# Optimization experiments

Hardware: AMD Instinct MI355X
Metric: run time of the kernel (lower is better)

Reference implementation:

```python
import jax, jax.numpy as jnp
import numpy as np

LEAK = 0.2

def leaky(x):
    return jnp.where(x > 0, x, LEAK * x)

def relu(x):
    return jnp.maximum(x, 0)

def conv1d(x, w):
    # x [B,Cin,L], w [Cout,Cin,3], stride 1, padding 1
    return jax.lax.conv_general_dilated(x, w, (1,), [(1, 1)],
        dimension_numbers=('NCH', 'OIH', 'NCH'))

def conv2d(x, w, pad, dil=1, groups=1):
    return jax.lax.conv_general_dilated(x, w, (1, 1), [(pad, pad), (pad, pad)],
        rhs_dilation=(dil, dil), feature_group_count=groups,
        dimension_numbers=('NCHW', 'OIHW', 'NCHW'))

def bn2d(x, p, eps=1e-5):
    # p: [4,C] = gamma, beta, running_mean, running_var (eval-mode BN)
    g, b, m, v = p
    s = (1, -1, 1, 1)
    return (x - m.reshape(s)) * (g.reshape(s) / jnp.sqrt(v.reshape(s) + eps)) + b.reshape(s)

def layernorm(x, g, b, eps=1e-5):
    mu = x.mean(-1, keepdims=True)
    var = ((x - mu) ** 2).mean(-1, keepdims=True)
    return (x - mu) / jnp.sqrt(var + eps) * g + b

def l2n(x, axis, eps):
    n = jnp.sqrt((x * x).sum(axis, keepdims=True))
    return x / jnp.maximum(n, eps)


def setup_inputs() -> dict:
    key = jax.random.key(0)
    B, C, H, W = 4, 64, 48, 48
    D, Fn, T, V = 256, 8, 4, 16
    E = 16  # orthogonal prototype embed dim
    ks = iter(jax.random.split(key, 64))
    def rn(shape, s=0.05):
        return jax.random.normal(next(ks), shape, jnp.float32) * s
    def bnp(c):
        return jnp.stack([1.0 + rn((c,), 0.1), rn((c,), 0.1), rn((c,), 0.1), 1.0 + jnp.abs(rn((c,), 0.1))])
    return dict(
        basis_vector_bank=jax.random.normal(next(ks), (T, V, D), jnp.float32),
        task_f=jax.random.normal(next(ks), (B, C, 16, 16), jnp.float32),
        img_f=jax.random.normal(next(ks), (B, C, H, W), jnp.float32),
        protos=jax.random.normal(next(ks), (T, E), jnp.float32),
        tA_w1=rn((E // 4, 1, 3)), tA_w2=rn((E // 2, E // 4, 3)),
        iA_w=rn((E // 2, C, 3, 3)), iA_bn=bnp(E // 2),
        at_w1=rn((E, Fn // 2 * E)), at_b1=rn((Fn // 2 * E,)),
        at_ln_g=jnp.ones((Fn // 2 * E,)), at_ln_b=jnp.zeros((Fn // 2 * E,)),
        at_w2=rn((Fn // 2 * E, Fn * E)), at_b2=rn((Fn * E,)),
        bv_t1=rn((D // 4, 1, 3)), bv_t2=rn((D // 2, D // 4, 3)),
        bv_ic1=rn((D // 4, C, 3, 3)), bv_bn1=bnp(D // 4),
        bv_ic2=rn((D // 2, D // 4, 3, 3)), bv_bn2=bnp(D // 2),
        bv_w1=rn((D, D // 4)), bv_b1=rn((D // 4,)),
        bv_ln_g=jnp.ones((D // 4,)), bv_ln_b=jnp.zeros((D // 4,)),
        bv_w2=rn((D // 4, D)), bv_b2=rn((D,)),
        m1_w1=rn((D, D // 4)), m1_b1=rn((D // 4,)),
        m1_ln_g=jnp.ones((D // 4,)), m1_ln_b=jnp.zeros((D // 4,)),
        m1_w2=rn((D // 4, C * C)), m1_b2=rn((C * C,)),
        m3_w1=rn((D, D // 4)), m3_b1=rn((D // 4,)),
        m3_ln_g=jnp.ones((D // 4,)), m3_ln_b=jnp.zeros((D // 4,)),
        m3_w2=rn((D // 4, 9 * C * C)), m3_b2=rn((9 * C * C,)),
        blr_bn=bnp(C),
        zc_w=rn((C, C, 1, 1), 0.01), zc_b=rn((C,), 0.01),
    )


def _forward(basis_vector_bank, task_f, img_f, protos, tA_w1, tA_w2, iA_w, iA_bn,
             at_w1, at_b1, at_ln_g, at_ln_b, at_w2, at_b2,
             bv_t1, bv_t2, bv_ic1, bv_bn1, bv_ic2, bv_bn2,
             bv_w1, bv_b1, bv_ln_g, bv_ln_b, bv_w2, bv_b2,
             m1_w1, m1_b1, m1_ln_g, m1_ln_b, m1_w2, m1_b2,
             m3_w1, m3_b1, m3_ln_g, m3_ln_b, m3_w2, m3_b2,
             blr_bn, zc_w, zc_b):
    T, V, D = basis_vector_bank.shape
    B, C, H, W = img_f.shape
    E = protos.shape[1]
    Fn = at_w2.shape[1] // E
    tau = 0.5

    # --- A2SI routing features ---
    xt = task_f.reshape(B, 1, -1)
    t1 = conv1d(leaky(conv1d(xt, tA_w1)), tA_w2).mean(-1)          # [B,E/2]
    i1 = leaky(bn2d(conv2d(img_f, iA_w, 1), iA_bn)).mean((2, 3))   # [B,E/2]
    f1 = jnp.concatenate([t1, i1], axis=1)                         # [B,E]
    h = relu(layernorm(f1 @ at_w1 + at_b1, at_ln_g, at_ln_b))
    tif = (h @ at_w2 + at_b2).reshape(B, E, Fn)                    # [B,E,F]
    logits = jnp.einsum('te,bef->bft', l2n(protos, -1, 1e-8), l2n(tif, 1, 1e-8))  # [B,F,T]

    # hard gumbel-softmax (straight-through), fixed noise key for determinism
    u = jax.random.uniform(jax.random.key(42), logits.shape, jnp.float32, 1e-10, 1.0)
    g = -jnp.log(-jnp.log(u))
    y = jax.nn.softmax((logits + g) / tau, axis=-1)
    idx = jnp.argmax(y, axis=-1)                                   # [B,F]
    y_hard = jax.nn.one_hot(idx, T, dtype=y.dtype)
    set_type = y_hard + y - jax.lax.stop_gradient(y)

    bank_flat = basis_vector_bank.reshape(T, V * D)
    sbvb = jnp.einsum('bft,tk->bfk', set_type, bank_flat).reshape(B, Fn, V, D)

    # --- BasisV_filter: filter feature ---
    xt2 = task_f.reshape(B, C, -1)
    rms = jnp.sqrt((xt2 ** 2).mean((1, 2), keepdims=True))
    xt2 = (xt2 / (rms + 1e-8)).reshape(B, 1, -1)
    te = conv1d(leaky(conv1d(xt2, bv_t1)), bv_t2).mean(-1)         # [B,D/2]
    ie = leaky(bn2d(conv2d(img_f, bv_ic1, 1), bv_bn1))
    ie = leaky(bn2d(conv2d(ie, bv_ic2, 1), bv_bn2)).mean((2, 3))   # [B,D/2]
    ff = jnp.concatenate([te, ie], axis=1)                         # [B,D]
    ff = relu(layernorm(ff @ bv_w1 + bv_b1, bv_ln_g, bv_ln_b)) @ bv_w2 + bv_b2

    # --- per-(batch,type) group gather/top-k/scatter, vectorized ---
    # group bank = bank of first filter with that type (hard one-hot -> type's bank)
    occ = idx[:, None, :] == jnp.arange(T)[None, :, None]          # [B,T,F]
    first = jnp.argmax(occ, axis=-1)                               # [B,T]
    Bg = jnp.take_along_axis(sbvb, first[:, :, None, None], axis=1)  # [B,T,V,D]
    # all rows of Q within a group are identical (filter_f expanded over F),
    # so S.max(0) == cosine(ff[b], Bg[b,t])
    scores = jnp.einsum('bd,btvd->btv', l2n(ff, -1, 1e-12), l2n(Bg, -1, 1e-12))
    order = jnp.argsort(-scores, axis=-1)                          # [B,T,V] topk order
    lt = jnp.tril(jnp.ones((Fn, Fn), bool), -1)                    # j < i
    rank = ((idx[:, :, None] == idx[:, None, :]) & lt).sum(-1)     # position in group
    bidx = jnp.arange(B)[:, None]
    sel = order[bidx, idx, rank]                                   # [B,F]
    bvf = Bg[bidx, idx, sel]                                       # [B,F,D]

    # --- per-filter dynamic convolutions ---
    w1 = relu(layernorm(bvf @ m1_w1 + m1_b1, m1_ln_g, m1_ln_b)) @ m1_w2 + m1_b2
    w1 = w1.reshape(B, Fn, C, C)                                   # [B,F,out,in]
    w3 = relu(layernorm(bvf @ m3_w1 + m3_b1, m3_ln_g, m3_ln_b)) @ m3_w2 + m3_b2
    w3 = w3.reshape(B * Fn, C, C, 3, 3)

    dp0 = jnp.einsum('bfoc,bchw->bfohw', w1, img_f)                # 1x1 branch
    xin = jnp.broadcast_to(img_f[:, None], (B, Fn, C, H, W)).reshape(1, B * Fn * C, H, W)
    ker = w3.reshape(B * Fn * C, C, 3, 3)
    dpd = [conv2d(xin, ker, d, dil=d, groups=B * Fn).reshape(B, Fn, C, H, W)
           for d in (1, 2, 3)]                                     # same-padded dilated 3x3
    t_ = idx[:, :, None, None, None]
    dp = jnp.where(t_ == 0, dp0, jnp.where(t_ == 1, dpd[0],
         jnp.where(t_ == 2, dpd[1], dpd[2])))                      # [B,F,C,H,W]

    x = leaky(bn2d(dp.reshape(B * Fn, C, H, W), blr_bn)).reshape(B, Fn, C, H, W).mean(1)
    a = conv2d(x, zc_w, 0) + zc_b.reshape(1, -1, 1, 1)
    return a + img_f


@jax.jit
def reference(basis_vector_bank, task_f, img_f, protos, tA_w1, tA_w2, iA_w, iA_bn,
              at_w1, at_b1, at_ln_g, at_ln_b, at_w2, at_b2,
              bv_t1, bv_t2, bv_ic1, bv_bn1, bv_ic2, bv_bn2,
              bv_w1, bv_b1, bv_ln_g, bv_ln_b, bv_w2, bv_b2,
              m1_w1, m1_b1, m1_ln_g, m1_ln_b, m1_w2, m1_b2,
              m3_w1, m3_b1, m3_ln_g, m3_ln_b, m3_w2, m3_b2,
              blr_bn, zc_w, zc_b):
    return _forward(basis_vector_bank, task_f, img_f, protos, tA_w1, tA_w2, iA_w, iA_bn,
                    at_w1, at_b1, at_ln_g, at_ln_b, at_w2, at_b2,
                    bv_t1, bv_t2, bv_ic1, bv_bn1, bv_ic2, bv_bn2,
                    bv_w1, bv_b1, bv_ln_g, bv_ln_b, bv_w2, bv_b2,
                    m1_w1, m1_b1, m1_ln_g, m1_ln_b, m1_w2, m1_b2,
                    m3_w1, m3_b1, m3_ln_g, m3_ln_b, m3_w2, m3_b2,
                    blr_bn, zc_w, zc_b)
```

## Files before the change

kernel.cpp:

```cpp
#include <hip/hip_runtime.h>
#include <math.h>

#define LEAKC 0.2f

#define NB 4
#define NC 64
#define LLEN 16384
#define HW 2304
#define PP 54
#define PHW 2916
#define SLABP 72
#define CP 72
#define IE1C 50

typedef __attribute__((ext_vector_type(8))) short short8;
typedef __attribute__((ext_vector_type(4))) float floatx4;

__device__ __forceinline__ float leaky(float x){ return x > 0.f ? x : LEAKC*x; }

__device__ __forceinline__ float wave_sum64(float v){
  for(int off=32;off;off>>=1) v += __shfl_xor(v,off);
  return v;
}

__device__ __forceinline__ unsigned short f2bf(float x){
  unsigned u=__float_as_uint(x);
  unsigned r=u+0x7FFFu+((u>>16)&1u);
  return (unsigned short)(r>>16);
}

__device__ __forceinline__ void threefry2x32(unsigned k0, unsigned k1, unsigned& x0, unsigned& x1){
  unsigned ks0=k0, ks1=k1, ks2=k0^k1^0x1BD11BDAu;
  x0+=ks0; x1+=ks1;
  const int rot0[4]={13,15,26,6};
  const int rot1[4]={17,29,16,24};
#define TF_APPLY(rr) {for(int r=0;r<4;r++){x0+=x1; x1=(x1<<rr[r])|(x1>>(32-rr[r])); x1^=x0;}}
  TF_APPLY(rot0); x0+=ks1; x1+=ks2+1u;
  TF_APPLY(rot1); x0+=ks2; x1+=ks0+2u;
  TF_APPLY(rot0); x0+=ks0; x1+=ks1+3u;
  TF_APPLY(rot1); x0+=ks1; x1+=ks2+4u;
  TF_APPLY(rot0); x0+=ks2; x1+=ks0+5u;
#undef TF_APPLY
}

__device__ __forceinline__ float jax_uniform128(int i){
  unsigned x0=0u, x1=(unsigned)i;
  threefry2x32(0u,42u,x0,x1);
  unsigned bits = x0 ^ x1;
  unsigned fb=(bits>>9)|0x3f800000u;
  float f=__uint_as_float(fb)-1.0f;
  float u=f*(1.0f-1e-10f)+1e-10f;
  return fmaxf(1e-10f,u);
}

__global__ __launch_bounds__(256) void k_pre(const float* __restrict__ task_f,
                      const float* __restrict__ w1A, const float* __restrict__ w1B,
                      float* __restrict__ totApart, float* __restrict__ a0A, float* __restrict__ aLA,
                      float* __restrict__ totBpart, float* __restrict__ a0B, float* __restrict__ aLB,
                      float* __restrict__ rmspart,
                      const float* __restrict__ img,
                      const float* __restrict__ w1, const float* __restrict__ w2,
                      const float* __restrict__ wa,
                      unsigned short* __restrict__ imgTP,
                      unsigned short* __restrict__ W1T, unsigned short* __restrict__ W2T,
                      unsigned short* __restrict__ WAT,
                      const float* __restrict__ mw1, const float* __restrict__ mw3,
                      const float* __restrict__ bvw1p, const float* __restrict__ bvw2p,
                      const float* __restrict__ bvt2p, const float* __restrict__ atw2p,
                      const float* __restrict__ bankp, float* __restrict__ warm){
  if(blockIdx.x<256){
    int b=blockIdx.x>>6, seg=blockIdx.x&63;
    const float* x=task_f+b*LLEN;
    float tA[4]={0,0,0,0};
    float tB[64];
#pragma unroll
    for(int c=0;c<64;c++) tB[c]=0.f;
    float sq=0.f;
    int l=seg*256+threadIdx.x;
    {
      float xm=(l>0)?x[l-1]:0.f;
      float xc=x[l];
      float xp=(l<LLEN-1)?x[l+1]:0.f;
      sq=xc*xc;
#pragma unroll
      for(int c=0;c<4;c++){
        float a=leaky(w1A[c*3+0]*xm + w1A[c*3+1]*xc + w1A[c*3+2]*xp);
        tA[c]=a;
        if(l==0) a0A[b*4+c]=a;
        if(l==LLEN-1) aLA[b*4+c]=a;
      }
#pragma unroll
      for(int c=0;c<64;c++){
        float a=leaky(w1B[c*3+0]*xm + w1B[c*3+1]*xc + w1B[c*3+2]*xp);
        tB[c]=a;
        if(l==0) a0B[b*64+c]=a;
        if(l==LLEN-1) aLB[b*64+c]=a;
      }
    }
    sq=wave_sum64(sq);
#pragma unroll
    for(int c=0;c<4;c++) tA[c]=wave_sum64(tA[c]);
#pragma unroll
    for(int c=0;c<64;c++){
      float v=tB[c];
      for(int off=32;off;off>>=1) v+=__shfl_down(v,off);
      tB[c]=v;
    }
    __shared__ float redB[4][64];
    __shared__ float redA[4][4];
    __shared__ float redQ[4];
    int wave=threadIdx.x>>6, lane=threadIdx.x&63;
    if(lane==0){
#pragma unroll
      for(int c=0;c<64;c++) redB[wave][c]=tB[c];
#pragma unroll
      for(int c=0;c<4;c++) redA[wave][c]=tA[c];
      redQ[wave]=sq;
    }
    __syncthreads();
    if(threadIdx.x<64){
      float s=redB[0][threadIdx.x]+redB[1][threadIdx.x]+redB[2][threadIdx.x]+redB[3][threadIdx.x];
      totBpart[(size_t)(b*64+seg)*64+threadIdx.x]=s;
    } else if(threadIdx.x<68){
      int c=threadIdx.x-64;
      totApart[(b*64+seg)*4+c]=redA[0][c]+redA[1][c]+redA[2][c]+redA[3][c];
    } else if(threadIdx.x==68){
      rmspart[b*64+seg]=redQ[0]+redQ[1]+redQ[2]+redQ[3];
    }
  } else if(blockIdx.x<400){
    int blk=blockIdx.x-256;
    int b=blk/36, t=blk%36;
    int p0=t*64;
    __shared__ float tile[64][65];
    int pp=threadIdx.x&63, c4=threadIdx.x>>6;
    for(int r=0;r<16;r++){
      int c=c4*16+r;
      tile[c][pp]=img[(b*64+c)*HW + p0+pp];
    }
    __syncthreads();
    int pxl=threadIdx.x>>2, cg=(threadIdx.x&3)*16;
    unsigned out[8];
#pragma unroll
    for(int q=0;q<8;q++){
      unsigned lo=f2bf(tile[cg+2*q][pxl]);
      unsigned hi=f2bf(tile[cg+2*q+1][pxl]);
      out[q]=lo|(hi<<16);
    }
    int px=p0+pxl;
    int h=px/48, w=px-h*48;
    int poff=(h+3)*PP+(w+3);
    unsigned* dst=(unsigned*)(imgTP + ((size_t)(b*PHW+poff))*64 + cg);
#pragma unroll
    for(int q=0;q<8;q++) dst[q]=out[q];
  } else if(blockIdx.x<868){
    int n=(blockIdx.x-400)*256+threadIdx.x;
    if(n<9*64*64){
      int tap=n>>12, oc=(n>>6)&63, c=n&63;
      W1T[n]=f2bf(w1[oc*576+c*9+tap]);
    } else if(n<9*64*64+9*128*64){
      int m=n-9*64*64;
      int tap=m/8192, r=m-tap*8192, oc=r>>6, c=r&63;
      W2T[m]=f2bf(w2[oc*576+c*9+tap]);
    } else {
      int q=n-9*64*64-9*128*64;
      if(q<9*16*64){
        int tap=q>>10, r=q&1023, o=r>>6, c=r&63;
        WAT[q]=(o<8)?f2bf(wa[o*576+c*9+tap]):(unsigned short)0;
      }
    }
  } else if(blockIdx.x<884){
    int t=(blockIdx.x-868)*256+threadIdx.x;
    float a=0.f;
    for(int i=t;i*16<16384;i+=4096) a+=mw1[i*16];
    for(int i=t;i*16<16384;i+=4096) a+=mw3[i*16];
    for(int i=t;i*16<16384;i+=4096) a+=bvw1p[i*16];
    for(int i=t;i*16<16384;i+=4096) a+=bvw2p[i*16];
    for(int i=t;i*16<24576;i+=4096) a+=bvt2p[i*16];
    for(int i=t;i*16<8192;i+=4096) a+=atw2p[i*16];
    for(int i=t;i*16<16384;i+=4096) a+=bankp[i*16];
    warm[t&1023]=a;
  } else {
    int id=(blockIdx.x-884)*256+threadIdx.x;
    uint4 z=make_uint4(0,0,0,0);
    for(int cch=id;cch<19584;cch+=4096){
      int ck=cch&7, pxid=cch>>3;
      int b=pxid/612, p=pxid-b*612;
      int h,w;
      if(p<324){ int r=p/54; w=p-r*54; h=(r<3)?r:(r+48); }
      else { int q=p-324; int r2=q/6; int cc=q-r2*6; h=3+r2; w=(cc<3)?cc:(cc+48); }
      *(uint4*)(imgTP + ((size_t)(b*PHW + h*PP + w))*64 + ck*8)=z;
    }
  }
}

__global__ __launch_bounds__(512) void k_conv12(const unsigned short* __restrict__ imgTP,
                        const unsigned short* __restrict__ W1T,
                        const unsigned short* __restrict__ W2T,
                        const unsigned short* __restrict__ WAT,
                        const float* __restrict__ bn1, const float* __restrict__ bn2,
                        const float* __restrict__ bnA,
                        float* __restrict__ iepart, float* __restrict__ i1part){
  int tid=threadIdx.x;
  int lane=tid&63, wv=tid>>6;
  int n0=lane&15, kg=lane>>4;
  if(blockIdx.x<96){
    int blk=blockIdx.x;
    int b=blk/24, hp=blk-b*24;
    int h0=hp*2;
    __shared__ unsigned short slab[6*54*SLABP];
    __shared__ unsigned short ie1[4*IE1C*CP];
    {
      const unsigned short* ibase=imgTP+((size_t)b*PHW+(size_t)(h0+1)*PP)*64;
      for(int e=tid;e<6*54*8;e+=512){
        int rr=e/(54*8), rem=e-rr*54*8, w=rem>>3, ck=rem&7;
        uint4 v=*(const uint4*)(ibase+((size_t)(rr*PP+w))*64+ck*8);
        *(uint4*)(slab+(rr*54+w)*SLABP+ck*8)=v;
      }
      if(tid<64){
        int br=tid>>4, cq=(tid>>3)&1, ck=tid&7;
        *(uint4*)(ie1+((size_t)(br*IE1C+(cq?49:0)))*CP+ck*8)=make_uint4(0,0,0,0);
      }
    }
    __syncthreads();
    {
      int mt=wv&3, rh=wv>>2;
      floatx4 acc[2][3];
#pragma unroll
      for(int rr=0;rr<2;rr++)
#pragma unroll
        for(int nt=0;nt<3;nt++) acc[rr][nt]=(floatx4){0.f,0.f,0.f,0.f};
#pragma unroll
      for(int ti=0;ti<3;ti++){
#pragma unroll
        for(int tj=0;tj<3;tj++){
          int tap=ti*3+tj;
          const unsigned short* Ab=W1T+(size_t)tap*4096;
#pragma unroll
          for(int c0=0;c0<64;c0+=32){
            short8 a=*(const short8*)(Ab+((mt*16+n0)*64+c0+kg*8));
#pragma unroll
            for(int rr=0;rr<2;rr++){
              int sr=rh*2+rr+ti;
#pragma unroll
              for(int nt=0;nt<3;nt++){
                int sc=nt*16+n0+tj+2;
                short8 bv=*(const short8*)(slab+(sr*54+sc)*SLABP+c0+kg*8);
                acc[rr][nt]=__builtin_amdgcn_mfma_f32_16x16x32_bf16(a,bv,acc[rr][nt],0,0,0);
              }
            }
          }
        }
      }
      int obase=mt*16+kg*4;
      float scale[4],m_[4],be_[4];
#pragma unroll
      for(int reg=0;reg<4;reg++){
        int o=obase+reg;
        scale[reg]=bn1[o]/sqrtf(bn1[192+o]+1e-5f);
        m_[reg]=bn1[128+o]; be_[reg]=bn1[64+o];
      }
#pragma unroll
      for(int rr=0;rr<2;rr++){
        int br=rh*2+rr;
        bool rv=((unsigned)(h0-1+br))<48u;
#pragma unroll
        for(int nt=0;nt<3;nt++){
          float v0=rv?leaky((acc[rr][nt][0]-m_[0])*scale[0]+be_[0]):0.f;
          float v1=rv?leaky((acc[rr][nt][1]-m_[1])*scale[1]+be_[1]):0.f;
          float v2=rv?leaky((acc[rr][nt][2]-m_[2])*scale[2]+be_[2]):0.f;
          float v3=rv?leaky((acc[rr][nt][3]-m_[3])*scale[3]+be_[3]):0.f;
          unsigned w0=f2bf(v0)|((unsigned)f2bf(v1)<<16);
          unsigned w1=f2bf(v2)|((unsigned)f2bf(v3)<<16);
          uint2 pk={w0,w1};
          *(uint2*)(ie1+((size_t)(br*IE1C+(nt*16+1+n0)))*CP+obase)=pk;
        }
      }
    }
    __syncthreads();
    {
      int mt2=wv;
      floatx4 acc[6];
#pragma unroll
      for(int i=0;i<6;i++) acc[i]=(floatx4){0.f,0.f,0.f,0.f};
#pragma unroll
      for(int ti=0;ti<3;ti++){
#pragma unroll
        for(int tj=0;tj<3;tj++){
          int tap=ti*3+tj;
          const unsigned short* Ab=W2T+(size_t)tap*8192;
#pragma unroll
          for(int c0=0;c0<64;c0+=32){
            short8 a=*(const short8*)(Ab+((mt2*16+n0)*64+c0+kg*8));
#pragma unroll
            for(int rr=0;rr<2;rr++){
              int sr=rr+ti;
#pragma unroll
              for(int wc=0;wc<3;wc++){
                int q=wc*16+n0+tj;
                short8 bv=*(const short8*)(ie1+((size_t)(sr*IE1C+q))*CP+c0+kg*8);
                acc[rr*3+wc]=__builtin_amdgcn_mfma_f32_16x16x32_bf16(a,bv,acc[rr*3+wc],0,0,0);
              }
            }
          }
        }
      }
      int obase=mt2*16+kg*4;
#pragma unroll
      for(int reg=0;reg<4;reg++){
        int o=obase+reg;
        float scale=bn2[o]/sqrtf(bn2[384+o]+1e-5f);
        float m_=bn2[256+o], be_=bn2[128+o];
        float part=0;
#pragma unroll
        for(int i=0;i<6;i++) part+=leaky((acc[i][reg]-m_)*scale+be_);
        for(int off=1;off<16;off<<=1) part+=__shfl_xor(part,off);
        if(n0==0) iepart[(b*24+hp)*128+o]=part*(1.f/2304.f);
      }
    }
  } else {
    int blk2=blockIdx.x-96;
    int b=blk2/3, hg=blk2-b*3;
    int hp=hg*8+wv;
    int h0=hp*2;
    const unsigned short* ib=imgTP+(size_t)b*PHW*64;
    floatx4 acc[6];
#pragma unroll
    for(int i=0;i<6;i++) acc[i]=(floatx4){0.f,0.f,0.f,0.f};
#pragma unroll
    for(int ti=0;ti<3;ti++){
#pragma unroll
      for(int tj=0;tj<3;tj++){
        int tap=ti*3+tj;
        const unsigned short* Ab=WAT+(size_t)tap*1024;
#pragma unroll
        for(int c0=0;c0<64;c0+=32){
          short8 a=*(const short8*)(Ab+(n0*64+c0+kg*8));
#pragma unroll
          for(int rr=0;rr<2;rr++){
            int r=h0+rr+ti-1+3;
#pragma unroll
            for(int wc=0;wc<3;wc++){
              int w=wc*16+n0+tj-1+3;
              short8 bv=*(const short8*)(ib+((size_t)(r*PP+w)*64+c0+kg*8));
              acc[rr*3+wc]=__builtin_amdgcn_mfma_f32_16x16x32_bf16(a,bv,acc[rr*3+wc],0,0,0);
            }
          }
        }
      }
    }
    int obase=kg*4;
#pragma unroll
    for(int reg=0;reg<4;reg++){
      int o=obase+reg;
      float part=0;
      if(o<8){
        float scale=bnA[o]/sqrtf(bnA[24+o]+1e-5f);
        float m_=bnA[16+o], be_=bnA[8+o];
#pragma unroll
        for(int i=0;i<6;i++) part+=leaky((acc[i][reg]-m_)*scale+be_);
      }
      for(int off=1;off<16;off<<=1) part+=__shfl_xor(part,off);
      if(n0==0 && o<8) i1part[(b*24+hp)*8+o]=part*(1.f/2304.f);
    }
  }
}

__global__ __launch_bounds__(512,1) void k_mid(
    const float* __restrict__ totApart, const float* __restrict__ a0A, const float* __restrict__ aLA,
    const float* __restrict__ totBpart, const float* __restrict__ a0B, const float* __restrict__ aLB,
    const float* __restrict__ rmspart,
    const float* __restrict__ tA_w2, const float* __restrict__ bv_t2,
    const float* __restrict__ i1part, const float* __restrict__ iepart,
    const float* __restrict__ at_w1, const float* __restrict__ at_b1,
    const float* __restrict__ at_ln_g, const float* __restrict__ at_ln_b,
    const float* __restrict__ at_w2, const float* __restrict__ at_b2,
    const float* __restrict__ protos,
    const float* __restrict__ bv_w1, const float* __restrict__ bv_b1,
    const float* __restrict__ bv_ln_g, const float* __restrict__ bv_ln_b,
    const float* __restrict__ bv_w2, const float* __restrict__ bv_b2,
    const float* __restrict__ bank,
    const float* __restrict__ m1_w1, const float* __restrict__ m1_b1,
    const float* __restrict__ m1_g,  const float* __restrict__ m1_bb,
    const float* __restrict__ m3_w1, const float* __restrict__ m3_b1,
    const float* __restrict__ m3_g,  const float* __restrict__ m3_bb,
    int* __restrict__ idxo, float* __restrict__ hid1, float* __restrict__ hid3){
  int b=blockIdx.x;
  int tid=threadIdx.x;
  int lane=tid&63, wv=tid>>6;
  const float invL=1.0f/16384.0f;
  __shared__ float sT[64], s0[64], sL[64];
  __shared__ float totA_s[4];
  __shared__ float rms_s;
  __shared__ float part[512];
  __shared__ float te_s[128], t1_s[8];
  __shared__ float f1[16], h[64], tif[128], tifn[128], tden[8], pden[4], pn[64], z[32];
  __shared__ int sidx[8], sfirst[4], srank[8], rows[8];
  __shared__ float fbuf[256], hh[64], ffn_s[256], finv_s;
  __shared__ float scores[64];
  __shared__ int order[64];
  __shared__ float bvf[2048];

  if(tid<64){
    float s=0;
#pragma unroll 8
    for(int seg=0;seg<64;seg++) s+=totBpart[(size_t)(b*64+seg)*64+tid];
    sT[tid]=s;
  } else if(tid<128){
    int t=tid-64;
    s0[t]=a0B[b*64+t]; sL[t]=aLB[b*64+t];
  } else if(tid<192){
    float v=rmspart[b*64+(tid-128)];
    v=wave_sum64(v);
    if(tid==128) rms_s=v;
  } else if(tid<256){
    int c=tid-192;
    if(c<4){
      float s=0;
#pragma unroll 8
      for(int seg=0;seg<64;seg++) s+=totApart[(b*64+seg)*4+c];
      totA_s[c]=s;
    }
  }
  __syncthreads();
  float scB=1.0f/(sqrtf(rms_s*invL)+1e-8f);
  if(tid<256){
    int c2=tid&127, h2=tid>>7;
    const float* wr=bv_t2+c2*192;
    float s=0;
    for(int c1=h2*32;c1<h2*32+32;c1+=8){
      float4 q[6];
      const float4* r4=(const float4*)(wr+c1*3);
#pragma unroll
      for(int u=0;u<6;u++) q[u]=r4[u];
      const float* qq=(const float*)q;
#pragma unroll
      for(int u=0;u<8;u++){
        int c=c1+u;
        float T=sT[c], A0=s0[c], AL=sL[c];
        s += qq[u*3+0]*(T-AL) + qq[u*3+1]*T + qq[u*3+2]*(T-A0);
      }
    }
    part[tid]=s;
  } else if(tid>=384 && tid<392){
    int c2=tid-384;
    float s=0;
    for(int c1=0;c1<4;c1++){
      float T=totA_s[c1], A0=a0A[b*4+c1], AL=aLA[b*4+c1];
      const float* w=&tA_w2[(c2*4+c1)*3];
      s += w[0]*(T-AL) + w[1]*T + w[2]*(T-A0);
    }
    t1_s[c2]=s*invL;
  }
  __syncthreads();
  if(tid<128) te_s[tid]=(part[tid]+part[tid+128])*invL*scB;
  __syncthreads();

  if(tid<8) f1[tid]=t1_s[tid];
  else if(tid<16){
    int f=tid-8;
    float s=0;
#pragma unroll
    for(int g=0;g<24;g++) s+=i1part[(b*24+g)*8+f];
    f1[tid]=s;
  }
  __syncthreads();
  if(tid<64){
    float s=at_b1[lane];
#pragma unroll
    for(int i=0;i<16;i++) s+=f1[i]*at_w1[i*64+lane];
    float mu=wave_sum64(s)*(1.f/64.f);
    float d=s-mu;
    float var=wave_sum64(d*d)*(1.f/64.f);
    h[lane]=fmaxf(d*(1.0f/sqrtf(var+1e-5f))*at_ln_g[lane]+at_ln_b[lane],0.f);
  }
  __syncthreads();
  if(tid<256){
    int n=tid&127, h2=tid>>7;
    float a0=0,a1=0;
    for(int k=h2*32;k<h2*32+32;k+=2){
      a0+=h[k]*at_w2[k*128+n];
      a1+=h[k+1]*at_w2[(k+1)*128+n];
    }
    part[tid]=a0+a1;
  }
  __syncthreads();
  if(tid<128) tif[tid]=at_b2[tid]+part[tid]+part[tid+128];
  __syncthreads();
  if(tid<8){
    int f=tid;
    float ss=0; for(int e=0;e<16;e++){float v=tif[e*8+f]; ss+=v*v;}
    tden[f]=fmaxf(sqrtf(ss),1e-8f);
  } else if(tid<12){
    int t=tid-8;
    float ss=0; for(int e=0;e<16;e++){float v=protos[t*16+e]; ss+=v*v;}
    pden[t]=fmaxf(sqrtf(ss),1e-8f);
  }
  __syncthreads();
  if(tid<128) tifn[tid]=tif[tid]/tden[tid&7];
  if(tid<64) pn[tid]=protos[tid]/pden[tid>>4];
  __syncthreads();
  if(tid<32){
    int f=tid>>2, t=tid&3;
    float ss=0;
#pragma unroll
    for(int e=0;e<16;e++) ss+=pn[t*16+e]*tifn[e*8+f];
    float u=jax_uniform128(b*32+f*4+t);
    float g=-logf(-logf(u));
    z[tid]=ss+g;
  }
  __syncthreads();
  if(tid<8){
    float best=z[tid*4]; int bi=0;
    for(int t=1;t<4;t++){ float v=z[tid*4+t]; if(v>best){best=v;bi=t;} }
    sidx[tid]=bi;
  }
  __syncthreads();
  if(tid<4){
    int t=tid;
    int fi=0;
    for(int f=7;f>=0;f--) if(sidx[f]==t) fi=f;
    sfirst[t]=fi;
  } else if(tid<12){
    int f=tid-4;
    int c=0; for(int f2=0;f2<f;f2++) if(sidx[f2]==sidx[f]) c++;
    srank[f]=c;
  }
  __syncthreads();

  if(tid<128) fbuf[tid]=te_s[tid];
  else if(tid<256){
    int c=tid-128;
    float s=0;
#pragma unroll 8
    for(int g=0;g<24;g++) s+=iepart[(b*24+g)*128+c];
    fbuf[tid]=s;
  }
  __syncthreads();
  if(tid<256){
    int l64=tid&63, q=tid>>6;
    float a0=0,a1=0,a2=0,a3=0;
    for(int k=q*64;k<q*64+64;k+=4){
      a0+=fbuf[k]  *bv_w1[k*64+l64];
      a1+=fbuf[k+1]*bv_w1[(k+1)*64+l64];
      a2+=fbuf[k+2]*bv_w1[(k+2)*64+l64];
      a3+=fbuf[k+3]*bv_w1[(k+3)*64+l64];
    }
    part[tid]=((a0+a1)+(a2+a3));
  }
  __syncthreads();
  if(tid<64){
    float s=bv_b1[lane]+part[lane]+part[64+lane]+part[128+lane]+part[192+lane];
    float mu=wave_sum64(s)*(1.f/64.f);
    float d=s-mu;
    float var=wave_sum64(d*d)*(1.f/64.f);
    hh[lane]=fmaxf(d*(1.0f/sqrtf(var+1e-5f))*bv_ln_g[lane]+bv_ln_b[lane],0.f);
  }
  __syncthreads();
  {
    int n=tid&255, h2=tid>>8;
    float a0=0,a1=0;
    for(int k=h2*32;k<h2*32+32;k+=2){
      a0+=hh[k]*bv_w2[k*256+n];
      a1+=hh[k+1]*bv_w2[(k+1)*256+n];
    }
    part[tid]=a0+a1;
  }
  __syncthreads();
  if(tid<256) ffn_s[tid]=bv_b2[tid]+part[tid]+part[tid+256];
  __syncthreads();
  if(tid<64){
    float sq=0;
#pragma unroll
    for(int u=0;u<4;u++){ float v=ffn_s[u*64+lane]; sq+=v*v; }
    sq=wave_sum64(sq);
    if(lane==0) finv_s=1.0f/fmaxf(sqrtf(sq),1e-12f);
  }
  __syncthreads();
  if(tid<256) ffn_s[tid]*=finv_s;
  __syncthreads();

  if(tid<128){
    int it=tid&63, h2=tid>>6;
    int t=it>>4, v=it&15;
    int tt=sidx[sfirst[t]];
    const float4* row=(const float4*)(bank+(tt*16+v)*256);
    float sa=0,na=0;
    for(int d4=h2*32;d4<h2*32+32;d4++){
      float4 r=row[d4];
      const float* fp=&ffn_s[d4*4];
      sa+=fp[0]*r.x+fp[1]*r.y+fp[2]*r.z+fp[3]*r.w;
      na+=r.x*r.x+r.y*r.y+r.z*r.z+r.w*r.w;
    }
    part[tid]=sa;
    part[256+tid]=na;
  }
  __syncthreads();
  if(tid<64) scores[tid]=(part[tid]+part[tid+64])/fmaxf(sqrtf(part[256+tid]+part[320+tid]),1e-12f);
  __syncthreads();
  if(tid<4){
    const float* sc=&scores[tid*16];
    unsigned used=0;
    for(int pk=0;pk<16;pk++){
      int best=-1; float bv=-1e30f;
      for(int v2=0;v2<16;v2++){
        if(used&(1u<<v2)) continue;
        float vv=sc[v2];
        if(best<0||vv>bv){bv=vv;best=v2;}
      }
      used|=1u<<best;
      order[tid*16+pk]=best;
    }
  }
  __syncthreads();
  if(tid<8){
    int t=sidx[tid];
    int v=order[t*16+srank[tid]];
    rows[tid]=t*16+v;
    idxo[b*8+tid]=t;
  }
  __syncthreads();

  for(int ii=tid;ii<2048;ii+=512){
    int r=ii>>8, d=ii&255;
    bvf[ii]=bank[rows[r]*256+d];
  }
  __syncthreads();
  {
    int r=wv;
    const float* bp=&bvf[r*256];
    float a0=0,a1=0,a2=0,a3=0;
    float c0=0,c1=0,c2=0,c3=0;
    for(int d=0;d<256;d+=4){
      float b0=bp[d],b1=bp[d+1],b2=bp[d+2],b3=bp[d+3];
      a0+=b0*m1_w1[d*64+lane];
      a1+=b1*m1_w1[(d+1)*64+lane];
      a2+=b2*m1_w1[(d+2)*64+lane];
      a3+=b3*m1_w1[(d+3)*64+lane];
      c0+=b0*m3_w1[d*64+lane];
      c1+=b1*m3_w1[(d+1)*64+lane];
      c2+=b2*m3_w1[(d+2)*64+lane];
      c3+=b3*m3_w1[(d+3)*64+lane];
    }
    float s1=m1_b1[lane]+((a0+a1)+(a2+a3));
    float s3=m3_b1[lane]+((c0+c1)+(c2+c3));
    float mu=wave_sum64(s1)*(1.f/64.f);
    float dd=s1-mu;
    float var=wave_sum64(dd*dd)*(1.f/64.f);
    hid1[(b*8+r)*64+lane]=fmaxf(dd*(1.0f/sqrtf(var+1e-5f))*m1_g[lane]+m1_bb[lane],0.f);
    mu=wave_sum64(s3)*(1.f/64.f);
    dd=s3-mu;
    var=wave_sum64(dd*dd)*(1.f/64.f);
    hid3[(b*8+r)*64+lane]=fmaxf(dd*(1.0f/sqrtf(var+1e-5f))*m3_g[lane]+m3_bb[lane],0.f);
  }
}

__global__ __launch_bounds__(256) void k_heads(const float* __restrict__ hid1, const float* __restrict__ hid3,
                        const float* __restrict__ w2a, const float* __restrict__ b2a,
                        const float* __restrict__ w2b, const float* __restrict__ b2b,
                        unsigned short* __restrict__ A1, unsigned short* __restrict__ A3){
  __shared__ float hl[2048];
  if(blockIdx.x<16){
    int n=blockIdx.x*256+threadIdx.x;
    for(int i=threadIdx.x;i<2048;i+=256) hl[i]=hid1[i];
    __syncthreads();
    float wcol[64];
#pragma unroll
    for(int k=0;k<64;k++) wcol[k]=w2a[k*4096+n];
    float bb=b2a[n];
    for(int bf=0;bf<32;bf++){
      float s=bb;
#pragma unroll
      for(int k=0;k<64;k++) s+=hl[bf*64+k]*wcol[k];
      A1[bf*4096+n]=f2bf(s);
    }
  } else {
    int n=(blockIdx.x-16)*256+threadIdx.x;
    for(int i=threadIdx.x;i<2048;i+=256) hl[i]=hid3[i];
    __syncthreads();
    float wcol[64];
#pragma unroll
    for(int k=0;k<64;k++) wcol[k]=w2b[(size_t)k*36864+n];
    float bb=b2b[n];
    int o=n/576, rem=n-o*576;
    int c=rem/9, tap=rem-c*9;
    size_t base=((size_t)tap*64+o)*64+c;
    for(int bf=0;bf<32;bf++){
      float s=bb;
#pragma unroll
      for(int k=0;k<64;k++) s+=hl[bf*64+k]*wcol[k];
      A3[(size_t)bf*9*4096+base]=f2bf(s);
    }
  }
}

__global__ __launch_bounds__(512) void k_dynF(const unsigned short* __restrict__ imgTP,
                       const unsigned short* __restrict__ A1, const unsigned short* __restrict__ A3,
                       const int* __restrict__ idx, const float* __restrict__ bn,
                       const float* __restrict__ zc_w, const float* __restrict__ zc_b,
                       const float* __restrict__ img, float* __restrict__ out){
  int blk=blockIdx.x;
  int b=blk/48, r0=blk-b*48;
  int tid=threadIdx.x;
  int lane=tid&63, w8=tid>>6;
  int mt=w8&3, fh=w8>>2;
  int n0=lane&15, kg=lane>>4;
  __shared__ unsigned short slab[7*54*SLABP];
  __shared__ float xl[64*50];
  __shared__ float zl[4096];
  for(int i=tid;i<4096;i+=512) zl[i]=zc_w[i];
  for(int i=tid;i<3200;i+=512) xl[i]=0.f;
  {
    const unsigned short* ibase=imgTP+((size_t)b*PHW+(size_t)r0*PP)*64;
    for(int e=tid;e<7*54*8;e+=512){
      int rr=e/(54*8), rem=e-rr*54*8, w=rem>>3, ck=rem&7;
      uint4 v=*(const uint4*)(ibase + ((size_t)(rr*PP+w))*64 + ck*8);
      *(uint4*)(slab + (rr*54+w)*SLABP + ck*8)=v;
    }
  }
  __syncthreads();
  int obase=mt*16+kg*4;
  float scale[4],m_[4],be_[4];
#pragma unroll
  for(int reg=0;reg<4;reg++){
    int o=obase+reg;
    scale[reg]=bn[o]/sqrtf(bn[192+o]+1e-5f);
    m_[reg]=bn[128+o]; be_[reg]=bn[64+o];
  }
  float xsum[3][4];
#pragma unroll
  for(int wc=0;wc<3;wc++)
#pragma unroll
    for(int reg=0;reg<4;reg++) xsum[wc][reg]=0.f;
  for(int f=fh*4;f<fh*4+4;f++){
    int bf=b*8+f;
    int tt=idx[bf];
    floatx4 acc[3];
#pragma unroll
    for(int i=0;i<3;i++) acc[i]=(floatx4){0.f,0.f,0.f,0.f};
    if(tt==0){
      const unsigned short* Ab=A1+(size_t)bf*4096;
#pragma unroll
      for(int c0=0;c0<64;c0+=32){
        short8 a=*(const short8*)(Ab+((mt*16+n0)*64+c0+kg*8));
#pragma unroll
        for(int wc=0;wc<3;wc++){
          short8 bv=*(const short8*)(slab + (3*54 + wc*16+n0+3)*SLABP + c0+kg*8);
          acc[wc]=__builtin_amdgcn_mfma_f32_16x16x32_bf16(a,bv,acc[wc],0,0,0);
        }
      }
    } else {
      int d=tt;
      const unsigned short* A3b=A3+(size_t)bf*9*4096;
#pragma unroll
      for(int ti=0;ti<3;ti++){
        int lr=d*(ti-1)+3;
#pragma unroll
        for(int tj=0;tj<3;tj++){
          int tap=ti*3+tj;
          int dw=d*(tj-1)+3;
          const unsigned short* Ab=A3b+(size_t)tap*4096;
#pragma unroll
          for(int c0=0;c0<64;c0+=32){
            short8 a=*(const short8*)(Ab+((mt*16+n0)*64+c0+kg*8));
#pragma unroll
            for(int wc=0;wc<3;wc++){
              short8 bv=*(const short8*)(slab + (lr*54 + wc*16+n0+dw)*SLABP + c0+kg*8);
              acc[wc]=__builtin_amdgcn_mfma_f32_16x16x32_bf16(a,bv,acc[wc],0,0,0);
            }
          }
        }
      }
    }
#pragma unroll
    for(int wc=0;wc<3;wc++)
#pragma unroll
      for(int reg=0;reg<4;reg++)
        xsum[wc][reg]+=leaky((acc[wc][reg]-m_[reg])*scale[reg]+be_[reg]);
  }
#pragma unroll
  for(int wc=0;wc<3;wc++)
#pragma unroll
    for(int reg=0;reg<4;reg++)
      atomicAdd(&xl[(obase+reg)*50 + wc*16+n0], xsum[wc][reg]*0.125f);
  __syncthreads();
  size_t base=(size_t)b*64*HW + r0*48;
  for(int e=tid;e<3072;e+=512){
    int o=e/48, px=e-o*48;
    float s=zc_b[o];
#pragma unroll
    for(int c=0;c<64;c++) s+=zl[o*64+c]*xl[c*50+px];
    size_t a=base+(size_t)o*HW+px;
    out[a]=s+img[a];
  }
}

extern "C" void kernel_launch(void* const* d_in, const int* in_sizes, int n_in,
                              void* d_out, int out_size, void* d_ws, size_t ws_size,
                              hipStream_t stream){
  const float* bank   =(const float*)d_in[0];
  const float* task_f =(const float*)d_in[1];
  const float* img_f  =(const float*)d_in[2];
  const float* protos =(const float*)d_in[3];
  const float* tA_w1  =(const float*)d_in[4];
  const float* tA_w2  =(const float*)d_in[5];
  const float* iA_w   =(const float*)d_in[6];
  const float* iA_bn  =(const float*)d_in[7];
  const float* at_w1  =(const float*)d_in[8];
  const float* at_b1  =(const float*)d_in[9];
  const float* at_ln_g=(const float*)d_in[10];
  const float* at_ln_b=(const float*)d_in[11];
  const float* at_w2  =(const float*)d_in[12];
  const float* at_b2  =(const float*)d_in[13];
  const float* bv_t1  =(const float*)d_in[14];
  const float* bv_t2  =(const float*)d_in[15];
  const float* bv_ic1 =(const float*)d_in[16];
  const float* bv_bn1 =(const float*)d_in[17];
  const float* bv_ic2 =(const float*)d_in[18];
  const float* bv_bn2 =(const float*)d_in[19];
  const float* bv_w1  =(const float*)d_in[20];
  const float* bv_b1  =(const float*)d_in[21];
  const float* bv_ln_g=(const float*)d_in[22];
  const float* bv_ln_b=(const float*)d_in[23];
  const float* bv_w2  =(const float*)d_in[24];
  const float* bv_b2  =(const float*)d_in[25];
  const float* m1_w1  =(const float*)d_in[26];
  const float* m1_b1  =(const float*)d_in[27];
  const float* m1_ln_g=(const float*)d_in[28];
  const float* m1_ln_b=(const float*)d_in[29];
  const float* m1_w2  =(const float*)d_in[30];
  const float* m1_b2  =(const float*)d_in[31];
  const float* m3_w1  =(const float*)d_in[32];
  const float* m3_b1  =(const float*)d_in[33];
  const float* m3_ln_g=(const float*)d_in[34];
  const float* m3_ln_b=(const float*)d_in[35];
  const float* m3_w2  =(const float*)d_in[36];
  const float* m3_b2  =(const float*)d_in[37];
  const float* blr_bn =(const float*)d_in[38];
  const float* zc_w   =(const float*)d_in[39];
  const float* zc_b   =(const float*)d_in[40];

  float* ws=(float*)d_ws;
  float* totApart=ws+0;
  float* a0A  =ws+1024;
  float* aLA  =ws+1040;
  float* totBpart=ws+1056;
  float* a0B  =ws+17440;
  float* aLB  =ws+17696;
  float* rmspart=ws+17952;
  float* i1part =ws+18208;
  float* iepart =ws+18976;
  int*   idxp   =(int*)(ws+31264);
  float* hid1=ws+31296;
  float* hid3=ws+33344;
  unsigned short* A1p  =(unsigned short*)(ws+35392);
  unsigned short* A3p  =(unsigned short*)(ws+100928);
  unsigned short* imgTP=(unsigned short*)(ws+690752);
  unsigned short* W1Tp =(unsigned short*)(ws+1064000);
  unsigned short* W2Tp =(unsigned short*)(ws+1082432);
  unsigned short* WATp =(unsigned short*)(ws+1119296);
  float* warm =ws+1123904;

  k_pre<<<900,256,0,stream>>>(task_f, tA_w1, bv_t1,
                              totApart, a0A, aLA, totBpart, a0B, aLB, rmspart,
                              img_f, bv_ic1, bv_ic2, iA_w, imgTP, W1Tp, W2Tp, WATp,
                              m1_w1, m3_w1, bv_w1, bv_w2, bv_t2, at_w2, bank, warm);
  k_conv12<<<108,512,0,stream>>>(imgTP, W1Tp, W2Tp, WATp, bv_bn1, bv_bn2, iA_bn,
                                 iepart, i1part);
  k_mid<<<4,512,0,stream>>>(totApart,a0A,aLA,totBpart,a0B,aLB, rmspart, tA_w2, bv_t2,
                            i1part, iepart,
                            at_w1, at_b1, at_ln_g, at_ln_b, at_w2, at_b2, protos,
                            bv_w1, bv_b1, bv_ln_g, bv_ln_b, bv_w2, bv_b2, bank,
                            m1_w1, m1_b1, m1_ln_g, m1_ln_b,
                            m3_w1, m3_b1, m3_ln_g, m3_ln_b,
                            idxp, hid1, hid3);
  k_heads<<<160,256,0,stream>>>(hid1, hid3, m1_w2, m1_b2, m3_w2, m3_b2, A1p, A3p);
  k_dynF<<<192,512,0,stream>>>(imgTP, A1p, A3p, idxp, blr_bn, zc_w, zc_b, img_f, (float*)d_out);

  (void)in_sizes; (void)n_in; (void)out_size; (void)ws_size;
}
```

Measured before the change: 267.2 us.

## Fuse preprocessing and conv kernels into one launch, converting weights inline

Merges the preprocessing kernel and the conv12 kernel into a single 512-thread kernel. The conv blocks now read img_f directly and convert it to a bf16 slab in shared memory, instead of reading the transposed imgTP buffer. Conv weights are converted from fp32 to bf16 on the fly inside the MFMA loops rather than pre-transposed in a separate pass. The iA conv is computed from the shared slab within the same blocks, with partials expanded to 6 per block. This removes one launch and the weight-transpose pass, at the cost of strided fp32 weight gathers and conversions in the inner loops. Both the pre and conv work now run in one grid, so the conv blocks no longer depend on imgTP.

```diff
diff --git a/kernel.cpp b/kernel.cpp
--- a/kernel.cpp
+++ b/kernel.cpp
@@ -53,30 +53,36 @@
   return fmaxf(1e-10f,u);
 }
 
-__global__ __launch_bounds__(256) void k_pre(const float* __restrict__ task_f,
-                      const float* __restrict__ w1A, const float* __restrict__ w1B,
-                      float* __restrict__ totApart, float* __restrict__ a0A, float* __restrict__ aLA,
-                      float* __restrict__ totBpart, float* __restrict__ a0B, float* __restrict__ aLB,
-                      float* __restrict__ rmspart,
-                      const float* __restrict__ img,
-                      const float* __restrict__ w1, const float* __restrict__ w2,
-                      const float* __restrict__ wa,
-                      unsigned short* __restrict__ imgTP,
-                      unsigned short* __restrict__ W1T, unsigned short* __restrict__ W2T,
-                      unsigned short* __restrict__ WAT,
-                      const float* __restrict__ mw1, const float* __restrict__ mw3,
-                      const float* __restrict__ bvw1p, const float* __restrict__ bvw2p,
-                      const float* __restrict__ bvt2p, const float* __restrict__ atw2p,
-                      const float* __restrict__ bankp, float* __restrict__ warm){
-  if(blockIdx.x<256){
-    int b=blockIdx.x>>6, seg=blockIdx.x&63;
+__global__ __launch_bounds__(512) void kP(
+    const float* __restrict__ task_f,
+    const float* __restrict__ w1A, const float* __restrict__ w1B,
+    float* __restrict__ totApart, float* __restrict__ a0A, float* __restrict__ aLA,
+    float* __restrict__ totBpart, float* __restrict__ a0B, float* __restrict__ aLB,
+    float* __restrict__ rmspart,
+    const float* __restrict__ img,
+    const float* __restrict__ w1, const float* __restrict__ w2, const float* __restrict__ wa,
+    unsigned short* __restrict__ imgTP,
+    const float* __restrict__ mw1, const float* __restrict__ mw3,
+    const float* __restrict__ bvw1p, const float* __restrict__ bvw2p,
+    const float* __restrict__ bvt2p, const float* __restrict__ atw2p,
+    const float* __restrict__ bankp, float* __restrict__ warm,
+    const float* __restrict__ bn1, const float* __restrict__ bn2, const float* __restrict__ bnA,
+    float* __restrict__ iepart, float* __restrict__ i1part6){
+  __shared__ __align__(16) char smraw[75456];
+  int tid=threadIdx.x;
+  int lane=tid&63, wv=tid>>6;
+  int n0=lane&15, kg=lane>>4;
+  int blk=blockIdx.x;
+
+  if(blk<128){
+    int b=blk>>5, half=tid>>8, seg=(blk&31)*2+half, t256=tid&255;
     const float* x=task_f+b*LLEN;
     float tA[4]={0,0,0,0};
     float tB[64];
 #pragma unroll
     for(int c=0;c<64;c++) tB[c]=0.f;
     float sq=0.f;
-    int l=seg*256+threadIdx.x;
+    int l=seg*256+t256;
     {
       float xm=(l>0)?x[l-1]:0.f;
       float xc=x[l];
@@ -106,39 +112,39 @@
       for(int off=32;off;off>>=1) v+=__shfl_down(v,off);
       tB[c]=v;
     }
-    __shared__ float redB[4][64];
-    __shared__ float redA[4][4];
-    __shared__ float redQ[4];
-    int wave=threadIdx.x>>6, lane=threadIdx.x&63;
+    float (*redB)[64]=(float(*)[64])smraw;
+    float (*redA)[4]=(float(*)[4])(smraw+2048);
+    float *redQ=(float*)(smraw+2048+128);
     if(lane==0){
 #pragma unroll
-      for(int c=0;c<64;c++) redB[wave][c]=tB[c];
-#pragma unroll
-      for(int c=0;c<4;c++) redA[wave][c]=tA[c];
-      redQ[wave]=sq;
+      for(int c=0;c<64;c++) redB[wv][c]=tB[c];
+#pragma unroll
+      for(int c=0;c<4;c++) redA[wv][c]=tA[c];
+      redQ[wv]=sq;
     }
     __syncthreads();
-    if(threadIdx.x<64){
-      float s=redB[0][threadIdx.x]+redB[1][threadIdx.x]+redB[2][threadIdx.x]+redB[3][threadIdx.x];
-      totBpart[(size_t)(b*64+seg)*64+threadIdx.x]=s;
-    } else if(threadIdx.x<68){
-      int c=threadIdx.x-64;
-      totApart[(b*64+seg)*4+c]=redA[0][c]+redA[1][c]+redA[2][c]+redA[3][c];
-    } else if(threadIdx.x==68){
-      rmspart[b*64+seg]=redQ[0]+redQ[1]+redQ[2]+redQ[3];
-    }
-  } else if(blockIdx.x<400){
-    int blk=blockIdx.x-256;
-    int b=blk/36, t=blk%36;
+    int w0=half*4;
+    if(t256<64){
+      float s=redB[w0][t256]+redB[w0+1][t256]+redB[w0+2][t256]+redB[w0+3][t256];
+      totBpart[(size_t)(b*64+seg)*64+t256]=s;
+    } else if(t256<68){
+      int c=t256-64;
+      totApart[(b*64+seg)*4+c]=redA[w0][c]+redA[w0+1][c]+redA[w0+2][c]+redA[w0+3][c];
+    } else if(t256==68){
+      rmspart[b*64+seg]=redQ[w0]+redQ[w0+1]+redQ[w0+2]+redQ[w0+3];
+    }
+  } else if(blk<200){
+    int j=blk-128, b=j/18, pr=j-b*18, half=tid>>8, t=pr*2+half, t256=tid&255;
+    float (*tile2)[64][65]=(float(*)[64][65])smraw;
+    float (*tile)[65]=tile2[half];
     int p0=t*64;
-    __shared__ float tile[64][65];
-    int pp=threadIdx.x&63, c4=threadIdx.x>>6;
+    int pp=t256&63, c4=t256>>6;
     for(int r=0;r<16;r++){
       int c=c4*16+r;
       tile[c][pp]=img[(b*64+c)*HW + p0+pp];
     }
     __syncthreads();
-    int pxl=threadIdx.x>>2, cg=(threadIdx.x&3)*16;
+    int pxl=t256>>2, cg=(t256&3)*16;
     unsigned out[8];
 #pragma unroll
     for(int q=0;q<8;q++){
@@ -152,24 +158,8 @@
     unsigned* dst=(unsigned*)(imgTP + ((size_t)(b*PHW+poff))*64 + cg);
 #pragma unroll
     for(int q=0;q<8;q++) dst[q]=out[q];
-  } else if(blockIdx.x<868){
-    int n=(blockIdx.x-400)*256+threadIdx.x;
-    if(n<9*64*64){
-      int tap=n>>12, oc=(n>>6)&63, c=n&63;
-      W1T[n]=f2bf(w1[oc*576+c*9+tap]);
-    } else if(n<9*64*64+9*128*64){
-      int m=n-9*64*64;
-      int tap=m/8192, r=m-tap*8192, oc=r>>6, c=r&63;
-      W2T[m]=f2bf(w2[oc*576+c*9+tap]);
-    } else {
-      int q=n-9*64*64-9*128*64;
-      if(q<9*16*64){
-        int tap=q>>10, r=q&1023, o=r>>6, c=r&63;
-        WAT[q]=(o<8)?f2bf(wa[o*576+c*9+tap]):(unsigned short)0;
-      }
-    }
-  } else if(blockIdx.x<884){
-    int t=(blockIdx.x-868)*256+threadIdx.x;
+  } else if(blk<208){
+    int t=(blk-200)*512+tid;
     float a=0.f;
     for(int i=t;i*16<16384;i+=4096) a+=mw1[i*16];
     for(int i=t;i*16<16384;i+=4096) a+=mw3[i*16];
@@ -179,8 +169,8 @@
     for(int i=t;i*16<8192;i+=4096) a+=atw2p[i*16];
     for(int i=t;i*16<16384;i+=4096) a+=bankp[i*16];
     warm[t&1023]=a;
-  } else {
-    int id=(blockIdx.x-884)*256+threadIdx.x;
+  } else if(blk<216){
+    int id=(blk-208)*512+tid;
     uint4 z=make_uint4(0,0,0,0);
     for(int cch=id;cch<19584;cch+=4096){
       int ck=cch&7, pxid=cch>>3;
@@ -190,36 +180,22 @@
       else { int q=p-324; int r2=q/6; int cc=q-r2*6; h=3+r2; w=(cc<3)?cc:(cc+48); }
       *(uint4*)(imgTP + ((size_t)(b*PHW + h*PP + w))*64 + ck*8)=z;
     }
-  }
-}
-
-__global__ __launch_bounds__(512) void k_conv12(const unsigned short* __restrict__ imgTP,
-                        const unsigned short* __restrict__ W1T,
-                        const unsigned short* __restrict__ W2T,
-                        const unsigned short* __restrict__ WAT,
-                        const float* __restrict__ bn1, const float* __restrict__ bn2,
-                        const float* __restrict__ bnA,
-                        float* __restrict__ iepart, float* __restrict__ i1part){
-  int tid=threadIdx.x;
-  int lane=tid&63, wv=tid>>6;
-  int n0=lane&15, kg=lane>>4;
-  if(blockIdx.x<96){
-    int blk=blockIdx.x;
-    int b=blk/24, hp=blk-b*24;
+  } else {
+    int cblk=blk-216;
+    int b=cblk/24, hp=cblk-b*24;
     int h0=hp*2;
-    __shared__ unsigned short slab[6*54*SLABP];
-    __shared__ unsigned short ie1[4*IE1C*CP];
-    {
-      const unsigned short* ibase=imgTP+((size_t)b*PHW+(size_t)(h0+1)*PP)*64;
-      for(int e=tid;e<6*54*8;e+=512){
-        int rr=e/(54*8), rem=e-rr*54*8, w=rem>>3, ck=rem&7;
-        uint4 v=*(const uint4*)(ibase+((size_t)(rr*PP+w))*64+ck*8);
-        *(uint4*)(slab+(rr*54+w)*SLABP+ck*8)=v;
-      }
-      if(tid<64){
-        int br=tid>>4, cq=(tid>>3)&1, ck=tid&7;
-        *(uint4*)(ie1+((size_t)(br*IE1C+(cq?49:0)))*CP+ck*8)=make_uint4(0,0,0,0);
-      }
+    unsigned short* slab=(unsigned short*)smraw;
+    unsigned short* ie1=(unsigned short*)(smraw+46656);
+    for(int g=tid; g<19200; g+=512){
+      int w50=g%50; int rc=g/50; int c=rc&63; int r=rc>>6;
+      int ir=h0-2+r, iw=w50-1;
+      float v=0.f;
+      if((unsigned)ir<48u && (unsigned)iw<48u) v=img[((size_t)(b*64+c))*HW + ir*48 + iw];
+      slab[(r*54 + w50+2)*SLABP + c]=f2bf(v);
+    }
+    if(tid<64){
+      int br=tid>>4, cq=(tid>>3)&1, ck=tid&7;
+      *(uint4*)(ie1+((size_t)(br*IE1C+(cq?49:0)))*CP+ck*8)=make_uint4(0,0,0,0);
     }
     __syncthreads();
     {
@@ -234,10 +210,12 @@
 #pragma unroll
         for(int tj=0;tj<3;tj++){
           int tap=ti*3+tj;
-          const unsigned short* Ab=W1T+(size_t)tap*4096;
+          const float* wbase=w1+(size_t)(mt*16+n0)*576+tap;
 #pragma unroll
           for(int c0=0;c0<64;c0+=32){
-            short8 a=*(const short8*)(Ab+((mt*16+n0)*64+c0+kg*8));
+            short8 a;
+#pragma unroll
+            for(int u=0;u<8;u++) a[u]=(short)f2bf(wbase[(c0+kg*8+u)*9]);
 #pragma unroll
             for(int rr=0;rr<2;rr++){
               int sr=rh*2+rr+ti;
@@ -270,13 +248,47 @@
           float v2=rv?leaky((acc[rr][nt][2]-m_[2])*scale[2]+be_[2]):0.f;
           float v3=rv?leaky((acc[rr][nt][3]-m_[3])*scale[3]+be_[3]):0.f;
           unsigned w0=f2bf(v0)|((unsigned)f2bf(v1)<<16);
-          unsigned w1=f2bf(v2)|((unsigned)f2bf(v3)<<16);
-          uint2 pk={w0,w1};
+          unsigned w1p=f2bf(v2)|((unsigned)f2bf(v3)<<16);
+          uint2 pk={w0,w1p};
           *(uint2*)(ie1+((size_t)(br*IE1C+(nt*16+1+n0)))*CP+obase)=pk;
         }
       }
     }
     __syncthreads();
+    if(wv<6){
+      int rr=wv/3, wc=wv-rr*3;
+      floatx4 acc=(floatx4){0.f,0.f,0.f,0.f};
+#pragma unroll
+      for(int ti=0;ti<3;ti++){
+#pragma unroll
+        for(int tj=0;tj<3;tj++){
+          int tap=ti*3+tj;
+#pragma unroll
+          for(int c0=0;c0<64;c0+=32){
+            short8 a;
+#pragma unroll
+            for(int u=0;u<8;u++){
+              int c=c0+kg*8+u;
+              a[u]=(n0<8)?(short)f2bf(wa[n0*576+c*9+tap]):(short)0;
+            }
+            short8 bv=*(const short8*)(slab+((rr+ti+1)*54 + wc*16+n0+tj+2)*SLABP + c0+kg*8);
+            acc=__builtin_amdgcn_mfma_f32_16x16x32_bf16(a,bv,acc,0,0,0);
+          }
+        }
+      }
+#pragma unroll
+      for(int reg=0;reg<4;reg++){
+        int o=kg*4+reg;
+        float part=0.f;
+        if(o<8){
+          float scale=bnA[o]/sqrtf(bnA[24+o]+1e-5f);
+          float m_=bnA[16+o], be_=bnA[8+o];
+          part=leaky((acc[reg]-m_)*scale+be_);
+        }
+        for(int off=1;off<16;off<<=1) part+=__shfl_xor(part,off);
+        if(n0==0 && o<8) i1part6[((b*24+hp)*6+wv)*8+o]=part*(1.f/2304.f);
+      }
+    }
     {
       int mt2=wv;
       floatx4 acc[6];
@@ -287,10 +299,12 @@
 #pragma unroll
         for(int tj=0;tj<3;tj++){
           int tap=ti*3+tj;
-          const unsigned short* Ab=W2T+(size_t)tap*8192;
+          const float* wbase2=w2+(size_t)(mt2*16+n0)*576+tap;
 #pragma unroll
           for(int c0=0;c0<64;c0+=32){
-            short8 a=*(const short8*)(Ab+((mt2*16+n0)*64+c0+kg*8));
+            short8 a;
+#pragma unroll
+            for(int u=0;u<8;u++) a[u]=(short)f2bf(wbase2[(c0+kg*8+u)*9]);
 #pragma unroll
             for(int rr=0;rr<2;rr++){
               int sr=rr+ti;
@@ -317,51 +331,6 @@
         if(n0==0) iepart[(b*24+hp)*128+o]=part*(1.f/2304.f);
       }
     }
-  } else {
-    int blk2=blockIdx.x-96;
-    int b=blk2/3, hg=blk2-b*3;
-    int hp=hg*8+wv;
-    int h0=hp*2;
-    const unsigned short* ib=imgTP+(size_t)b*PHW*64;
-    floatx4 acc[6];
-#pragma unroll
-    for(int i=0;i<6;i++) acc[i]=(floatx4){0.f,0.f,0.f,0.f};
-#pragma unroll
-    for(int ti=0;ti<3;ti++){
-#pragma unroll
-      for(int tj=0;tj<3;tj++){
-        int tap=ti*3+tj;
-        const unsigned short* Ab=WAT+(size_t)tap*1024;
-#pragma unroll
-        for(int c0=0;c0<64;c0+=32){
-          short8 a=*(const short8*)(Ab+(n0*64+c0+kg*8));
-#pragma unroll
-          for(int rr=0;rr<2;rr++){
-            int r=h0+rr+ti-1+3;
-#pragma unroll
-            for(int wc=0;wc<3;wc++){
-              int w=wc*16+n0+tj-1+3;
-              short8 bv=*(const short8*)(ib+((size_t)(r*PP+w)*64+c0+kg*8));
-              acc[rr*3+wc]=__builtin_amdgcn_mfma_f32_16x16x32_bf16(a,bv,acc[rr*3+wc],0,0,0);
-            }
-          }
-        }
-      }
-    }
-    int obase=kg*4;
-#pragma unroll
-    for(int reg=0;reg<4;reg++){
-      int o=obase+reg;
-      float part=0;
-      if(o<8){
-        float scale=bnA[o]/sqrtf(bnA[24+o]+1e-5f);
-        float m_=bnA[16+o], be_=bnA[8+o];
-#pragma unroll
-        for(int i=0;i<6;i++) part+=leaky((acc[i][reg]-m_)*scale+be_);
-      }
-      for(int off=1;off<16;off<<=1) part+=__shfl_xor(part,off);
-      if(n0==0 && o<8) i1part[(b*24+hp)*8+o]=part*(1.f/2304.f);
-    }
   }
 }
 
@@ -370,7 +339,7 @@
     const float* __restrict__ totBpart, const float* __restrict__ a0B, const float* __restrict__ aLB,
     const float* __restrict__ rmspart,
     const float* __restrict__ tA_w2, const float* __restrict__ bv_t2,
-    const float* __restrict__ i1part, const float* __restrict__ iepart,
+    const float* __restrict__ i1part6, const float* __restrict__ iepart,
     const float* __restrict__ at_w1, const float* __restrict__ at_b1,
     const float* __restrict__ at_ln_g, const float* __restrict__ at_ln_b,
     const float* __restrict__ at_w2, const float* __restrict__ at_b2,
@@ -459,8 +428,7 @@
   else if(tid<16){
     int f=tid-8;
     float s=0;
-#pragma unroll
-    for(int g=0;g<24;g++) s+=i1part[(b*24+g)*8+f];
+    for(int g=0;g<144;g++) s+=i1part6[(b*144+g)*8+f];
     f1[tid]=s;
   }
   __syncthreads();
@@ -847,27 +815,25 @@
   float* a0B  =ws+17440;
   float* aLB  =ws+17696;
   float* rmspart=ws+17952;
-  float* i1part =ws+18208;
-  float* iepart =ws+18976;
-  int*   idxp   =(int*)(ws+31264);
-  float* hid1=ws+31296;
-  float* hid3=ws+33344;
-  unsigned short* A1p  =(unsigned short*)(ws+35392);
-  unsigned short* A3p  =(unsigned short*)(ws+100928);
-  unsigned short* imgTP=(unsigned short*)(ws+690752);
-  unsigned short* W1Tp =(unsigned short*)(ws+1064000);
-  unsigned short* W2Tp =(unsigned short*)(ws+1082432);
-  unsigned short* WATp =(unsigned short*)(ws+1119296);
-  float* warm =ws+1123904;
-
-  k_pre<<<900,256,0,stream>>>(task_f, tA_w1, bv_t1,
-                              totApart, a0A, aLA, totBpart, a0B, aLB, rmspart,
-                              img_f, bv_ic1, bv_ic2, iA_w, imgTP, W1Tp, W2Tp, WATp,
-                              m1_w1, m3_w1, bv_w1, bv_w2, bv_t2, at_w2, bank, warm);
-  k_conv12<<<108,512,0,stream>>>(imgTP, W1Tp, W2Tp, WATp, bv_bn1, bv_bn2, iA_bn,
-                                 iepart, i1part);
+  float* i1part6=ws+18208;
+  float* iepart =ws+22816;
+  int*   idxp   =(int*)(ws+35104);
+  float* hid1=ws+35136;
+  float* hid3=ws+37184;
+  unsigned short* A1p  =(unsigned short*)(ws+39232);
+  unsigned short* A3p  =(unsigned short*)(ws+104768);
+  unsigned short* imgTP=(unsigned short*)(ws+694592);
+  float* warm =ws+1067840;
+
+  kP<<<312,512,0,stream>>>(task_f, tA_w1, bv_t1,
+                           totApart, a0A, aLA, totBpart, a0B, aLB, rmspart,
+                           img_f, bv_ic1, bv_ic2, iA_w,
+                           imgTP,
+                           m1_w1, m3_w1, bv_w1, bv_w2, bv_t2, at_w2, bank, warm,
+                           bv_bn1, bv_bn2, iA_bn,
+                           iepart, i1part6);
   k_mid<<<4,512,0,stream>>>(totApart,a0A,aLA,totBpart,a0B,aLB, rmspart, tA_w2, bv_t2,
-                            i1part, iepart,
+                            i1part6, iepart,
                             at_w1, at_b1, at_ln_g, at_ln_b, at_w2, at_b2, protos,
                             bv_w1, bv_b1, bv_ln_g, bv_ln_b, bv_w2, bv_b2, bank,
                             m1_w1, m1_b1, m1_ln_g, m1_ln_b,
```

New measurement: 317.0 us. 1.19x slower.
